# Optimization experiments

Measured on AMD Instinct MI355X. Metric: run time of the kernel, lower is better.

Reference implementation:

```python
import math
import jax, jax.numpy as jnp
from jax import lax
import numpy as np

N_IMG = 2
C = 128
IMG_H, IMG_W = 512, 1024
STRIDES = (4, 8, 16, 32, 64)
SIZES = (32.0, 64.0, 128.0, 256.0, 512.0)
RATIOS = (0.5, 1.0, 2.0)
A = len(RATIOS)
PRE_NMS_TOPK = 2000    # pre_nms_topk[self.training] with training=True
POST_NMS_TOPK = 1000   # post_nms_topk[self.training]
NMS_THRESH = 0.7
BATCH_PER_IMG = 256
POS_FRAC = 0.5
MIN_BOX_SIZE = 0.0
SCALE_CLAMP = math.log(1000.0 / 16.0)
MATCH_LOW, MATCH_HIGH = 0.3, 0.7


def cell_anchors(size):
    rs = jnp.asarray(RATIOS, jnp.float32)
    area = size * size
    w = jnp.sqrt(area / rs)
    h = w * rs
    return jnp.stack([-w / 2, -h / 2, w / 2, h / 2], axis=1)  # [A,4]


def level_anchors(H, W, stride, size):
    ca = cell_anchors(size)
    sx = jnp.arange(W, dtype=jnp.float32) * stride
    sy = jnp.arange(H, dtype=jnp.float32) * stride
    yy, xx = jnp.meshgrid(sy, sx, indexing="ij")
    shifts = jnp.stack([xx, yy, xx, yy], axis=-1).reshape(-1, 4)  # [H*W,4]
    return (shifts[:, None, :] + ca[None, :, :]).reshape(-1, 4)  # [H*W*A,4]


def pairwise_iou(a, b):
    lt = jnp.maximum(a[:, None, :2], b[None, :, :2])
    rb = jnp.minimum(a[:, None, 2:], b[None, :, 2:])
    wh = jnp.clip(rb - lt, 0.0)
    inter = wh[..., 0] * wh[..., 1]
    area_a = (a[:, 2] - a[:, 0]) * (a[:, 3] - a[:, 1])
    area_b = (b[:, 2] - b[:, 0]) * (b[:, 3] - b[:, 1])
    union = area_a[:, None] + area_b[None, :] - inter
    return jnp.where(inter > 0, inter / union, 0.0)


def get_deltas(src, tgt):
    sw = src[..., 2] - src[..., 0]; sh = src[..., 3] - src[..., 1]
    scx = src[..., 0] + 0.5 * sw;   scy = src[..., 1] + 0.5 * sh
    tw = tgt[..., 2] - tgt[..., 0]; th = tgt[..., 3] - tgt[..., 1]
    tcx = tgt[..., 0] + 0.5 * tw;   tcy = tgt[..., 1] + 0.5 * th
    return jnp.stack([(tcx - scx) / sw, (tcy - scy) / sh,
                      jnp.log(tw / sw), jnp.log(th / sh)], axis=-1)


def apply_deltas(deltas, boxes):
    w = boxes[..., 2] - boxes[..., 0]; h = boxes[..., 3] - boxes[..., 1]
    cx = boxes[..., 0] + 0.5 * w;      cy = boxes[..., 1] + 0.5 * h
    dx, dy = deltas[..., 0], deltas[..., 1]
    dw = jnp.minimum(deltas[..., 2], SCALE_CLAMP)
    dh = jnp.minimum(deltas[..., 3], SCALE_CLAMP)
    pcx = dx * w + cx; pcy = dy * h + cy
    pw = jnp.exp(dw) * w; ph = jnp.exp(dh) * h
    return jnp.stack([pcx - 0.5 * pw, pcy - 0.5 * ph,
                      pcx + 0.5 * pw, pcy + 0.5 * ph], axis=-1)


def conv(x, w, b):
    y = lax.conv_general_dilated(x, w, (1, 1), "SAME",
                                 dimension_numbers=("NCHW", "OIHW", "NCHW"))
    return y + b[None, :, None, None]


def rpn_forward_flat(feats, conv_w, conv_b, obj_w, obj_b, delta_w, delta_b):
    anchors, logits, deltas = [], [], []
    for (stride, size), f in zip(zip(STRIDES, SIZES), feats):
        N, _, H, W = f.shape
        h = jax.nn.relu(conv(f, conv_w, conv_b))
        lg = conv(h, obj_w, obj_b)       # [N,A,H,W]
        dl = conv(h, delta_w, delta_b)   # [N,4A,H,W]
        logits.append(lg.transpose(0, 2, 3, 1).reshape(N, -1))                     # [N,HWA]
        deltas.append(dl.reshape(N, A, 4, H, W).transpose(0, 3, 4, 1, 2).reshape(N, -1, 4))
        anchors.append(level_anchors(H, W, stride, size))
    return anchors, logits, deltas


def label_and_sample(gt_b, key, anchors_all):
    iou = pairwise_iou(gt_b, anchors_all)                 # [G,R]
    matched_idxs = jnp.argmax(iou, axis=0)
    matched_vals = jnp.max(iou, axis=0)
    labels = jnp.where(matched_vals >= MATCH_HIGH, 1,
             jnp.where(matched_vals >= MATCH_LOW, -1, 0))
    highest = jnp.max(iou, axis=1)                        # per-gt best IoU
    lq = jnp.any((iou == highest[:, None]) & (highest[:, None] > 0), axis=0)
    labels = jnp.where(lq, 1, labels)                     # allow_low_quality_matches
    R = labels.shape[0]
    kf, kb = jax.random.split(key)
    fg = labels == 1; bg = labels == 0
    num_fg = jnp.minimum(fg.sum(), int(POS_FRAC * BATCH_PER_IMG))
    num_bg = jnp.minimum(bg.sum(), BATCH_PER_IMG - num_fg)
    def pick(mask, k, num):
        pri = jnp.where(mask, jax.random.uniform(k, (R,)), jnp.inf)
        rank = jnp.argsort(jnp.argsort(pri))
        return rank < num
    sel_fg = pick(fg, kf, num_fg)
    sel_bg = pick(bg, kb, num_bg)
    labels = jnp.where(sel_fg, 1, jnp.where(sel_bg, 0, -1))
    return labels, gt_b[matched_idxs]


def losses_fn(anchors_all, logits_cat, deltas_cat, gt_labels, matched_gt):
    fg = (gt_labels == 1).astype(logits_cat.dtype)          # [N,R]
    gt_deltas = get_deltas(anchors_all[None], matched_gt)   # [N,R,4]
    loc = jnp.sum(jnp.abs(deltas_cat - gt_deltas) * fg[..., None])  # smooth_l1, beta=0
    valid = (gt_labels >= 0).astype(logits_cat.dtype)
    x = logits_cat
    bce = jnp.maximum(x, 0.0) - x * fg + jnp.log1p(jnp.exp(-jnp.abs(x)))
    cls = jnp.sum(bce * valid)
    norm = float(BATCH_PER_IMG) * logits_cat.shape[0]
    return jnp.stack([cls / norm, loc / norm])


def nms_keep(boxes, valid):
    # boxes are sorted by descending score; greedy suppression.
    K = boxes.shape[0]
    iou = pairwise_iou(boxes, boxes)
    idx = jnp.arange(K)
    def body(i, keep):
        sup = (iou[i] > NMS_THRESH) & (idx > i) & keep[i]
        return keep & ~sup
    return lax.fori_loop(0, K, body, valid)


def predict_proposals(anchors, logits, deltas):
    lvl_boxes, lvl_scores = [], []
    for anc, lg, dl in zip(anchors, logits, deltas):
        boxes = apply_deltas(dl, anc[None])             # [N,R_l,4]
        k = min(PRE_NMS_TOPK, lg.shape[1])
        ts, ti = lax.top_k(lg, k)                       # [N,k]
        tb = jnp.take_along_axis(boxes, ti[..., None], axis=1)
        tb = jnp.stack([jnp.clip(tb[..., 0], 0.0, IMG_W), jnp.clip(tb[..., 1], 0.0, IMG_H),
                        jnp.clip(tb[..., 2], 0.0, IMG_W), jnp.clip(tb[..., 3], 0.0, IMG_H)], -1)
        valid = ((tb[..., 2] - tb[..., 0]) > MIN_BOX_SIZE) & ((tb[..., 3] - tb[..., 1]) > MIN_BOX_SIZE)
        keep = jax.vmap(nms_keep)(tb, valid)
        lvl_boxes.append(tb)
        lvl_scores.append(jnp.where(keep, ts, -jnp.inf))
    all_b = jnp.concatenate(lvl_boxes, axis=1)
    all_s = jnp.concatenate(lvl_scores, axis=1)
    fs, fi = lax.top_k(all_s, POST_NMS_TOPK)
    fb = jnp.take_along_axis(all_b, fi[..., None], axis=1)
    return fb, fs


def setup_inputs() -> dict:
    key = jax.random.key(0)
    ks = jax.random.split(key, 12)
    out = {}
    for i, s in enumerate(STRIDES):
        out[f"feat_p{i+2}"] = jax.random.normal(ks[i], (N_IMG, C, IMG_H // s, IMG_W // s), jnp.float32)
    G = 32
    wh_scale = jnp.asarray([IMG_W, IMG_H], jnp.float32)
    cxy = jax.random.uniform(ks[5], (N_IMG, G, 2)) * wh_scale
    wh = 32.0 + jax.random.uniform(ks[6], (N_IMG, G, 2)) * 224.0
    x1y1 = jnp.clip(cxy - wh / 2, 0.0)
    x2y2 = jnp.maximum(jnp.minimum(cxy + wh / 2, wh_scale), x1y1 + 1.0)
    out["gt_boxes"] = jnp.concatenate([x1y1, x2y2], axis=-1)
    out["conv_w"] = 0.01 * jax.random.normal(ks[7], (C, C, 3, 3), jnp.float32)
    out["conv_b"] = jnp.zeros((C,), jnp.float32)
    out["obj_w"] = 0.01 * jax.random.normal(ks[8], (A, C, 1, 1), jnp.float32)
    out["obj_b"] = jnp.zeros((A,), jnp.float32)
    out["delta_w"] = 0.01 * jax.random.normal(ks[9], (4 * A, C, 1, 1), jnp.float32)
    out["delta_b"] = jnp.zeros((4 * A,), jnp.float32)
    return out


def reference(feat_p2, feat_p3, feat_p4, feat_p5, feat_p6, gt_boxes,
              conv_w, conv_b, obj_w, obj_b, delta_w, delta_b):
    feats = [feat_p2, feat_p3, feat_p4, feat_p5, feat_p6]
    anchors, logits, deltas = rpn_forward_flat(feats, conv_w, conv_b, obj_w, obj_b, delta_w, delta_b)
    anchors_all = jnp.concatenate(anchors, axis=0)      # [R,4]
    logits_cat = jnp.concatenate(logits, axis=1)        # [N,R]
    deltas_cat = jnp.concatenate(deltas, axis=1)        # [N,R,4]
    keys = jax.random.split(jax.random.key(42), gt_boxes.shape[0])
    gt_labels, matched_gt = jax.vmap(label_and_sample, in_axes=(0, 0, None))(gt_boxes, keys, anchors_all)
    losses = losses_fn(anchors_all, logits_cat, deltas_cat, gt_labels, matched_gt)
    prop_boxes, prop_scores = predict_proposals(
        anchors,
        [lax.stop_gradient(l) for l in logits],
        [lax.stop_gradient(d) for d in deltas])
    return prop_boxes, prop_scores, losses
```

## Files before the change

### kernel.cpp

```cpp
#include <hip/hip_runtime.h>
#include <stdint.h>
#include <math.h>


#define R_TOT   130944
#define HALF_R  65472
#define TOTK    7920
#define SCALE_CLAMP 4.135166556742356

__host__ __device__ inline void threefry(uint32_t k0, uint32_t k1,
                                         uint32_t x0, uint32_t x1,
                                         uint32_t* o0, uint32_t* o1)
{
  uint32_t ks[3]; ks[0]=k0; ks[1]=k1; ks[2]=k0^k1^0x1BD11BDAu;
  x0 += ks[0]; x1 += ks[1];
  const uint32_t rot0[4] = {13u,15u,26u,6u};
  const uint32_t rot1[4] = {17u,29u,16u,24u};
  for (int i = 0; i < 5; i++){
    const uint32_t* rot = (i & 1) ? rot1 : rot0;
    for (int q = 0; q < 4; q++){
      x0 += x1;
      x1 = (x1 << rot[q]) | (x1 >> (32u - rot[q]));
      x1 ^= x0;
    }
    x0 += ks[(i+1)%3];
    x1 += ks[(i+2)%3] + (uint32_t)(i+1);
  }
  *o0 = x0; *o1 = x1;
}

__device__ inline unsigned long long mono64(double v){
  unsigned long long b = (unsigned long long)__double_as_longlong(v);
  return (b & 0x8000000000000000ull) ? ~b : (b | 0x8000000000000000ull);
}

__device__ __forceinline__ double iou_cf(double g0,double g1,double g2,double g3,
                                         double a0,double a1,double a2,double a3){
  #pragma clang fp contract(off)
  double lt0 = fmax(g0,a0), lt1 = fmax(g1,a1);
  double rb0 = fmin(g2,a2), rb1 = fmin(g3,a3);
  double w = rb0-lt0; if (w<0.0) w=0.0;
  double h = rb1-lt1; if (h<0.0) h=0.0;
  double inter = w*h;
  double aa = (g2-g0)*(g3-g1);
  double ab = (a2-a0)*(a3-a1);
  double uni = aa+ab-inter;
  return inter>0.0 ? inter/uni : 0.0;
}

__device__ __forceinline__ void anchor_of(int r, double* o){
  #pragma clang fp contract(off)
  const int    base[5]={0,98304,122880,129024,130560};
  const int    Wl[5]  ={256,128,64,32,16};
  const double strd[5]={4.0,8.0,16.0,32.0,64.0};
  const double size[5]={32.0,64.0,128.0,256.0,512.0};
  const double ratio[3]={0.5,1.0,2.0};
  int l=0; while (l<4 && r>=base[l+1]) l++;
  int rr=r-base[l]; int pix=rr/3; int a=rr-pix*3;
  int x=pix%Wl[l], y=pix/Wl[l];
  double w=sqrt(size[l]*size[l]/ratio[a]);
  double h=w*ratio[a];
  double sx=(double)x*strd[l], sy=(double)y*strd[l];
  o[0]=sx-0.5*w; o[1]=sy-0.5*h; o[2]=sx+0.5*w; o[3]=sy+0.5*h;
}

__device__ __forceinline__ void decode_box(int ridx, const double* __restrict__ d,
                                           double* __restrict__ o){
  double a[4]; anchor_of(ridx,a);
  double w=a[2]-a[0], h=a[3]-a[1];
  double cx=a[0]+0.5*w, cy=a[1]+0.5*h;
  double dw=fmin(d[2],SCALE_CLAMP), dh=fmin(d[3],SCALE_CLAMP);
  double pcx=d[0]*w+cx, pcy=d[1]*h+cy;
  double pw=exp(dw)*w, ph=exp(dh)*h;
  double x1=pcx-0.5*pw, y1=pcy-0.5*ph;
  double x2=pcx+0.5*pw, y2=pcy+0.5*ph;
  o[0]=fmin(fmax(x1,0.0),1024.0); o[1]=fmin(fmax(y1,0.0),512.0);
  o[2]=fmin(fmax(x2,0.0),1024.0); o[3]=fmin(fmax(y2,0.0),512.0);
}

__device__ inline void bitonic_desc(double* sv, int* si, int M, int tid, int nthr){
  for (int k=2;k<=M;k<<=1)
    for (int j=k>>1;j>0;j>>=1){
      __syncthreads();
      for (int i=tid;i<M;i+=nthr){
        int ixj=i^j;
        if (ixj>i){
          double va=sv[i], vb=sv[ixj]; int ia=si[i], ib=si[ixj];
          bool before = (va>vb) || (va==vb && ia<ib);
          bool up = ((i&k)==0);
          if (up ? !before : before){ sv[i]=vb; sv[ixj]=va; si[i]=ib; si[ixj]=ia; }
        }
      }
    }
  __syncthreads();
}

__device__ inline void bitonic_asc_u(uint32_t* sk, int* si, int M, int tid, int nthr){
  for (int k=2;k<=M;k<<=1)
    for (int j=k>>1;j>0;j>>=1){
      __syncthreads();
      for (int i=tid;i<M;i+=nthr){
        int ixj=i^j;
        if (ixj>i){
          uint32_t ka=sk[i], kb=sk[ixj]; int ia=si[i], ib=si[ixj];
          bool before = (ka<kb) || (ka==kb && ia<ib);
          bool up = ((i&k)==0);
          if (up ? !before : before){ sk[i]=kb; sk[ixj]=ka; si[i]=ib; si[ixj]=ia; }
        }
      }
    }
  __syncthreads();
}

__device__ inline void hist_select(int* hist, int kneed, int tid,
                                   int* shb, int* shk){
  for (int off=1; off<256; off<<=1){
    int v=0;
    if (tid<256 && tid>=off) v=hist[tid-off];
    __syncthreads();
    if (tid<256) hist[tid]+=v;
    __syncthreads();
  }
  if (tid<256){
    int prev = tid ? hist[tid-1] : 0;
    if (prev < kneed && kneed <= hist[tid]){ *shb=tid; *shk=kneed-prev; }
    if (tid==255 && kneed > hist[255]){ *shb=255; *shk=kneed-hist[254]; }
  }
  __syncthreads();
}

__global__ __launch_bounds__(256) void k_pre(const float* __restrict__ cw,
    float* __restrict__ cwTf, const float* __restrict__ gt,
    unsigned long long* __restrict__ highest)
{
  const int bx=blockIdx.x, tid=threadIdx.x;
  if (bx < 576){
    int o = bx*256 + tid;
    if (o >= 147456) return;
    int cc = o & 127; int t = o >> 7;
    int k9 = t % 9;  int ci = t / 9;
    cwTf[(size_t)(ci*9+k9)*128 + cc] = cw[(size_t)cc*1152 + ci*9 + k9];
  } else {
    __shared__ double gts[128];
    __shared__ unsigned long long lmax[32];
    const int gb=bx-576;
    const int img=gb>>6, b=gb&63;
    if (tid<128) gts[tid]=(double)gt[img*128+tid];
    if (tid<32) lmax[tid]=0ull;
    __syncthreads();
    double gm[32];
    #pragma unroll
    for (int g=0;g<32;g++) gm[g]=0.0;
    for (int r=b*256+tid; r<R_TOT; r+=64*256){
      double a[4]; anchor_of(r,a);
      #pragma unroll
      for (int g=0;g<32;g++){
        double v=iou_cf(gts[g*4],gts[g*4+1],gts[g*4+2],gts[g*4+3],a[0],a[1],a[2],a[3]);
        gm[g]=fmax(gm[g],v);
      }
    }
    #pragma unroll
    for (int g=0;g<32;g++){
      double v=gm[g];
      #pragma unroll
      for (int off=1; off<64; off<<=1) v=fmax(v,__shfl_xor(v,off));
      if ((tid&63)==0) atomicMax(&lmax[g],(unsigned long long)__double_as_longlong(v));
    }
    __syncthreads();
    if (tid<32) atomicMax(&highest[img*32+tid], lmax[tid]);
  }
}

#define CTH 4
#define CTW 8

__global__ __launch_bounds__(256,4) void k_conv_label(
    const float* __restrict__ f2, const float* __restrict__ f3,
    const float* __restrict__ f4, const float* __restrict__ f5,
    const float* __restrict__ f6,
    const float* __restrict__ cwTf, const float* __restrict__ cb,
    const float* __restrict__ ow, const float* __restrict__ ob,
    const float* __restrict__ dwt, const float* __restrict__ dbt,
    double* __restrict__ logits, double* __restrict__ dpred,
    const float* __restrict__ gt, const unsigned long long* __restrict__ highest,
    int* __restrict__ prelab, int* __restrict__ matched,
    int* __restrict__ labels, int* __restrict__ counts,
    uint32_t* __restrict__ ub,
    uint32_t kf00,uint32_t kf01,uint32_t kb00,uint32_t kb01,
    uint32_t kf10,uint32_t kf11,uint32_t kb10,uint32_t kb11)
{
  __shared__ double fshd[4][6][12];
  __shared__ __align__(16) char ush[18432];
  float*  wshF = (float*)ush;
  double* hshp = (double*)ush;
  __shared__ float hw[15*128];
  __shared__ float hb[15];

  const int tid=threadIdx.x;
  const int vbid = blockIdx.x;

  if (vbid >= 3752){
    int j = (vbid-3752)*256 + tid;
    if (j >= 2*R_TOT) return;
    int slot = j / HALF_R; int t = j - slot*HALF_R;
    uint32_t k0,k1;
    if      (slot==0){k0=kf00;k1=kf01;}
    else if (slot==1){k0=kb00;k1=kb01;}
    else if (slot==2){k0=kf10;k1=kf11;}
    else             {k0=kb10;k1=kb11;}
    uint32_t o0,o1;
    threefry(k0,k1,(uint32_t)t,(uint32_t)(t+HALF_R),&o0,&o1);
    ub[(size_t)slot*R_TOT+t]=o0;
    ub[(size_t)slot*R_TOT+t+HALF_R]=o1;
    return;
  }

  if (vbid >= 2728){
    double* gts=(double*)ush;
    double* hg =(double*)(ush+1024);
    int* wfg=(int*)(ush+1280); int* wbg=(int*)(ush+1296);
    const int lb=vbid-2728;
    const int img=lb>>9, blk=lb&511;
    if (tid<128) gts[tid]=(double)gt[img*128+tid];
    if (tid<32)  hg[tid]=__longlong_as_double((long long)highest[img*32+tid]);
    __syncthreads();
    int r=blk*256+tid;
    const bool ok=(r<R_TOT);
    int lab=-1, bi=0;
    if (ok){
      double a[4]; anchor_of(r,a);
      double best=-1.0; bool lq=false;
      #pragma unroll
      for (int g=0;g<32;g++){
        double v=iou_cf(gts[g*4],gts[g*4+1],gts[g*4+2],gts[g*4+3],a[0],a[1],a[2],a[3]);
        if (v>best){ best=v; bi=g; }
        if (hg[g]>0.0 && v==hg[g]) lq=true;
      }
      lab = lq ? 1 : (best>=0.7 ? 1 : (best>=0.3 ? -1 : 0));
      prelab [(size_t)img*R_TOT+r]=lab;
      matched[(size_t)img*R_TOT+r]=bi;
      labels [(size_t)img*R_TOT+r]=-1;
    }
    unsigned long long bf=__ballot(ok && lab==1);
    unsigned long long bb=__ballot(ok && lab==0);
    const int wid=tid>>6, lane=tid&63;
    if (lane==0){ wfg[wid]=__popcll(bf); wbg[wid]=__popcll(bb); }
    __syncthreads();
    if (tid==0){
      int fcnt=wfg[0]+wfg[1]+wfg[2]+wfg[3];
      int bcnt=wbg[0]+wbg[1]+wbg[2]+wbg[3];
      if (fcnt) atomicAdd(&counts[img*2+0],fcnt);
      if (bcnt) atomicAdd(&counts[img*2+1],bcnt);
    }
    return;
  }

  const int cumt[6]={0,2048,2560,2688,2720,2728};
  const int Hs[5]={128,64,32,16,8}, Wl[5]={256,128,64,32,16};
  const int rbs[5]={0,98304,122880,129024,130560};
  const int lgx[5]={5,4,3,2,1};

  int bid=vbid;
  int lvl=0;
  while (lvl<4 && bid>=cumt[lvl+1]) lvl++;
  int t=bid-cumt[lvl];
  const int img=t&1; const int tt=t>>1;
  const int H=Hs[lvl], W=Wl[lvl], rbase=rbs[lvl];
  const int tx=tt&((1<<lgx[lvl])-1), ty=tt>>lgx[lvl];
  const int x0=tx*CTW, y0=ty*CTH;
  const float* f = lvl==0?f2: lvl==1?f3: lvl==2?f4: lvl==3?f5: f6;

  for (int i=tid;i<15*128;i+=256){
    int o=i>>7, c=i&127;
    hw[i]=(o<3)?ow[o*128+c]:dwt[(o-3)*128+c];
  }
  if (tid<15) hb[tid]=(tid<3)?ob[tid]:dbt[tid-3];

  const int c=tid&127, half=tid>>7;
  double acc[16];
  #pragma unroll
  for (int i=0;i<16;i++) acc[i]=0.0;

  const float* fimg = f + (size_t)img*128*H*W;

  const bool fin_act = (tid < 240);
  int ci_f=0,dy_f=0,dx_f=0; bool fin_valid=false;
  const float* fptr=fimg;
  if (fin_act){
    ci_f=tid/60; int rem=tid-ci_f*60; dy_f=rem/10; dx_f=rem-dy_f*10;
    int y=y0-1+dy_f, x=x0-1+dx_f;
    fin_valid = (y>=0&&y<H&&x>=0&&x<W);
    fptr = fimg + (size_t)ci_f*H*W + (fin_valid ? ((size_t)y*W+x) : 0);
  }
  const size_t fstep=(size_t)4*H*W;
  const float2* wsrc=(const float2*)cwTf;

  float fin_pf=0.f; float2 wpf[9];
  if (fin_act){ fin_pf = fin_valid ? *fptr : 0.f; fptr += fstep; }
  #pragma unroll
  for (int j2=0;j2<9;j2++) wpf[j2]=wsrc[tid+j2*256];

  for (int ci0=0; ci0<128; ci0+=4){
    __syncthreads();
    if (fin_act) fshd[ci_f][dy_f][dx_f]=(double)fin_pf;
    { float2* wdst=(float2*)wshF;
      #pragma unroll
      for (int j2=0;j2<9;j2++) wdst[tid+j2*256]=wpf[j2]; }
    if (ci0+4<128){
      if (fin_act){ fin_pf = fin_valid ? *fptr : 0.f; fptr += fstep; }
      const float2* wn = wsrc + (size_t)(ci0+4)*576;
      #pragma unroll
      for (int j2=0;j2<9;j2++) wpf[j2]=wn[tid+j2*256];
    }
    __syncthreads();
    #pragma unroll
    for (int ci=0;ci<4;ci++){
      double w9d[9];
      #pragma unroll
      for (int k=0;k<9;k++) w9d[k]=(double)wshF[(ci*9+k)*128 + c];
      #pragma unroll
      for (int irl=0;irl<4;irl++){
        int ir=half*2+irl;
        double rowb[10];
        #pragma unroll
        for (int q=0;q<10;q++) rowb[q]=fshd[ci][ir][q];
        #pragma unroll
        for (int orl=0;orl<2;orl++){
          int ky=irl-orl;
          if (ky<0||ky>2) continue;
          #pragma unroll
          for (int px=0;px<8;px++){
            double s=acc[orl*8+px];
            #pragma unroll
            for (int kx=0;kx<3;kx++) s += w9d[ky*3+kx]*rowb[px+kx];
            acc[orl*8+px]=s;
          }
        }
      }
    }
  }
  double bc=(double)cb[c];
  __syncthreads();
  if (half==0){
    #pragma unroll
    for (int pp=0;pp<16;pp++){
      double hv=acc[pp]+bc; if (hv<0.0) hv=0.0;
      hshp[c*17+pp]=hv;
    }
  }
  __syncthreads();
  for (int hp=0;hp<2;hp++){
    if (tid<240){
      int o=tid>>4, p=tid&15;
      double s=(double)hb[o];
      for (int c2=0;c2<128;c2++) s += (double)hw[o*128+c2]*hshp[c2*17+p];
      int pg=hp*16+p;
      int py=pg>>3, px=pg&7;
      int gy=y0+py, gx=x0+px;
      long long pix=(long long)gy*W+gx;
      size_t rb=(size_t)rbase+(size_t)pix*3;
      if (o<3) logits[(size_t)img*R_TOT+rb+o]=s;
      else { int a=(o-3)>>2, jj=(o-3)&3; dpred[((size_t)img*R_TOT+rb+a)*4+jj]=s; }
    }
    if (hp==0){
      __syncthreads();
      if (half==1){
        #pragma unroll
        for (int pp=0;pp<16;pp++){
          double hv=acc[pp]+bc; if (hv<0.0) hv=0.0;
          hshp[c*17+pp]=hv;
        }
      }
      __syncthreads();
    }
  }
}

__global__ __launch_bounds__(1024) void k_mid2(const uint32_t* __restrict__ ub,
    const int* __restrict__ prelab, const int* __restrict__ counts,
    int* __restrict__ labels,
    const double* __restrict__ logits, const double* __restrict__ dpred,
    double* __restrict__ allS, double* __restrict__ allB,
    unsigned long long* __restrict__ keepbuf,
    const float* __restrict__ gt, const int* __restrict__ matched,
    double* __restrict__ part, int* __restrict__ flags)
{
  __shared__ __align__(16) char buf[49152];
  __shared__ int hist[256];
  __shared__ int sI0, sI1;
  __shared__ int cnt;
  const int tid=threadIdx.x;

  if (blockIdx.x < 4){
    uint32_t* skey=(uint32_t*)buf; int* sidx=(int*)(buf+16384);
    const int img=blockIdx.x>>1, cls=blockIdx.x&1;
    const int cfg=counts[img*2+0], cbg=counts[img*2+1];
    const int num_fg=cfg<128?cfg:128;
    const int cap_bg=256-num_fg;
    const int num=cls?(cbg<cap_bg?cbg:cap_bg):num_fg;
    if (num<=0){
      if (tid==0){ __threadfence(); atomicAdd(&flags[13],1); }
      return;
    }
    const int want=cls?0:1;
    const int sel=want;
    const uint32_t* u=ub+(size_t)(img*2+cls)*R_TOT;
    const int* pl=prelab+(size_t)img*R_TOT;
    int* lab=labels+(size_t)img*R_TOT;

    for (int b=tid;b<256;b+=1024) hist[b]=0;
    if (tid==0) cnt=0;
    __syncthreads();
    #pragma unroll 4
    for (int r=tid;r<R_TOT;r+=1024){
      int plr = pl[r];
      uint32_t key = u[r]>>9;
      if (plr==want) atomicAdd(&hist[key>>15],1);
    }
    __syncthreads();
    hist_select(hist, num, tid, &sI0, &sI1);
    const uint32_t bsel=(uint32_t)sI0; const int kneed=sI1;
    #pragma unroll 4
    for (int r=tid;r<R_TOT;r+=1024){
      int plr = pl[r];
      uint32_t key = u[r]>>9;
      if (plr==want){
        uint32_t t8=key>>15;
        if (t8<bsel) lab[r]=sel;
        else if (t8==bsel){ int p=atomicAdd(&cnt,1); if (p<4096){ skey[p]=key; sidx[p]=r; } }
      }
    }
    __syncthreads();
    int n=cnt<4096?cnt:4096;
    for (int i=tid;i<4096;i+=1024) if (i>=n){ skey[i]=0xFFFFFFFFu; sidx[i]=0x7FFFFFFF; }
    bitonic_asc_u(skey,sidx,4096,tid,1024);
    int take = kneed<n?kneed:n;
    for (int i=tid;i<take;i+=1024) lab[sidx[i]]=sel;
    __syncthreads();
    if (tid==0){ __threadfence(); atomicAdd(&flags[13],1); }
  } else if (blockIdx.x < 14){
    double* sv=(double*)buf; int* si=(int*)(buf+32768);
    const int Rl[5]   ={98304,24576,6144,1536,384};
    const int kl[5]   ={2000,2000,2000,1536,384};
    const int lbase[5]={0,98304,122880,129024,130560};
    const int loff[5] ={0,2000,4000,6000,7536};
    const int bb=blockIdx.x-4;
    const int lvl=bb%5, img=bb/5;
    if (lvl==0 && tid<124) keepbuf[img*124+tid]=~0ull;
    const int Rn=Rl[lvl], K=kl[lvl];
    const double* lg=logits+(size_t)img*R_TOT+lbase[lvl];

    unsigned long long chosen=0; int kneed=K;
    for (int ps=7; ps>=6; --ps){
      int shift=ps*8;
      for (int b=tid;b<256;b+=1024) hist[b]=0;
      __syncthreads();
      #pragma unroll 4
      for (int r=tid;r<Rn;r+=1024){
        unsigned long long ik=~mono64(lg[r]);
        bool okp=(ps==7)||((ik>>(shift+8))==(chosen>>(shift+8)));
        if (okp) atomicAdd(&hist[(int)((ik>>shift)&255)],1);
      }
      __syncthreads();
      hist_select(hist, kneed, tid, &sI0, &sI1);
      chosen = chosen | ((unsigned long long)sI0<<shift);
      kneed  = sI1;
      __syncthreads();
    }
    const unsigned long long lim = chosen | 0xFFFFFFFFFFFFull;
    if (tid==0) cnt=0;
    __syncthreads();
    #pragma unroll 4
    for (int r=tid;r<Rn;r+=1024){
      unsigned long long ik=~mono64(lg[r]);
      if (ik<=lim){ int p=atomicAdd(&cnt,1); if (p<4096){ sv[p]=lg[r]; si[p]=r; } }
    }
    __syncthreads();
    int n=cnt<4096?cnt:4096;
    for (int i=tid;i<4096;i+=1024) if (i>=n){ sv[i]=-HUGE_VAL; si[i]=0x7FFFFFFF; }
    bitonic_desc(sv,si,4096,tid,1024);
    for (int j=tid;j<K;j+=1024){
      double v=sv[j]; int r=si[j];
      size_t slot=(size_t)img*TOTK+loff[lvl]+j;
      allS[slot]=v;
      int ridx=lbase[lvl]+r;
      double bx[4];
      decode_box(ridx, dpred+((size_t)img*R_TOT+ridx)*4, bx);
      allB[slot*4+0]=bx[0]; allB[slot*4+1]=bx[1]; allB[slot*4+2]=bx[2]; allB[slot*4+3]=bx[3];
    }
  } else {
    double* sc=(double*)buf; double* sl=(double*)(buf+8192);
    const int lb=blockIdx.x-14;
    if (tid==0){
      while (atomicAdd(&flags[13],0) < 4) __builtin_amdgcn_s_sleep(8);
    }
    __syncthreads();
    __threadfence();
    double cls=0.0, loc=0.0;
    for (int idx=lb*1024+tid; idx<2*R_TOT; idx+=64*1024){
      int l=labels[idx];
      if (l<0) continue;
      double x=logits[idx];
      double fgv=(l==1)?1.0:0.0;
      cls += fmax(x,0.0)-x*fgv+log1p(exp(-fabs(x)));
      if (l==1){
        int img=idx/R_TOT, r=idx-img*R_TOT;
        double a[4]; anchor_of(r,a);
        int m=matched[idx];
        const float* g=gt+img*128+m*4;
        double sw=a[2]-a[0], sh=a[3]-a[1];
        double scx=a[0]+0.5*sw, scy=a[1]+0.5*sh;
        double tw=(double)g[2]-(double)g[0], th=(double)g[3]-(double)g[1];
        double tcx=(double)g[0]+0.5*tw, tcy=(double)g[1]+0.5*th;
        double d0=(tcx-scx)/sw, d1=(tcy-scy)/sh;
        double d2=log(tw/sw), d3=log(th/sh);
        const double* dp=dpred+(size_t)idx*4;
        loc += fabs(dp[0]-d0)+fabs(dp[1]-d1)+fabs(dp[2]-d2)+fabs(dp[3]-d3);
      }
    }
    sc[tid]=cls; sl[tid]=loc; __syncthreads();
    for (int s=512;s>0;s>>=1){
      if (tid<s){ sc[tid]+=sc[tid+s]; sl[tid]+=sl[tid+s]; }
      __syncthreads();
    }
    if (tid==0){
      part[lb*2]=sc[0]; part[lb*2+1]=sl[0];
      __threadfence();
      atomicAdd(&flags[12],1);
    }
  }
}

__global__ __launch_bounds__(1024) void k_mid3post(const double* __restrict__ allB,
    unsigned long long* __restrict__ msk,
    double* __restrict__ part,
    const double* __restrict__ allS, int* __restrict__ flags,
    unsigned long long* __restrict__ keepbuf, float* __restrict__ out)
{
  __shared__ __align__(16) char ush[64000];
  const int tid=threadIdx.x, bx=blockIdx.x;
  const int kl[5]  ={2000,2000,2000,1536,384};
  const int loff[5]={0,2000,4000,6000,7536};
  const int MBLK[5]={63,63,63,48,12};

  if (bx < 10){
    if (tid >= 64) return;
    const int lvl=bx%5, img=bx/5;
    const int K=kl[lvl], off=loff[lvl], nw=(K+63)>>6;
    const int lane=tid;
    {
      const int target=MBLK[lvl];
      while (true){
        int v = (lane==0) ? atomicAdd(&flags[img*5+lvl],0) : 0;
        v = __shfl(v,0);
        if (v>=target) break;
        __builtin_amdgcn_s_sleep(8);
      }
      __threadfence();
    }
    const double* B=allB+(size_t)(img*TOTK+off)*4;
    const unsigned long long* M=msk+((size_t)img*TOTK+off)*32;
    unsigned long long keepw=0ull;
    if (lane<nw){
      for (int b=0;b<64;b++){
        int j=lane*64+b;
        if (j<K){
          double x1=B[(size_t)j*4],y1=B[(size_t)j*4+1],x2=B[(size_t)j*4+2],y2=B[(size_t)j*4+3];
          if ((x2-x1)>0.0 && (y2-y1)>0.0) keepw|=(1ull<<b);
        }
      }
    }
    for (int w=0; w<nw; w++){
      unsigned long long vw = __shfl(keepw, w);
      int row = w*64 + lane;
      unsigned long long mrow = (row<K) ? M[(size_t)row*32+w] : 0ull;
      unsigned long long m_lo = lane ? (mrow & ((1ull<<lane)-1ull)) : 0ull;
      const bool validL = (vw>>lane)&1ull;
      unsigned long long kmask = vw;
      while (true){
        bool s = validL && ((m_lo & kmask)==0ull);
        unsigned long long nk = __ballot(s);
        if (nk==kmask) break;
        kmask = nk;
      }
      if (lane==w) keepw = kmask;
      if (lane>w && lane<nw){
        unsigned long long sup=0ull;
        for (int b=0;b<64;b++){
          if ((kmask>>b)&1ull) sup |= M[(size_t)(w*64+b)*32+lane];
        }
        keepw &= ~sup;
      }
    }
    if (lane<nw){
      int nvalid = K - lane*64; if (nvalid>64) nvalid=64;
      unsigned long long vm = (nvalid>=64) ? ~0ull : ((1ull<<nvalid)-1ull);
      unsigned long long cbits = (~keepw) & vm;
      int gbase = off + lane*64;
      int w0 = gbase>>6, sh = gbase&63;
      unsigned long long* kb = keepbuf + (size_t)img*124;
      if (sh==0){
        if (cbits) atomicAnd(&kb[w0], ~cbits);
      } else {
        unsigned long long lo = cbits << sh;
        unsigned long long hi = cbits >> (64-sh);
        if (lo) atomicAnd(&kb[w0],   ~lo);
        if (hi) atomicAnd(&kb[w0+1], ~hi);
      }
    }
    __threadfence();
    if (tid==0) atomicAdd(&flags[10+img],1);
    return;
  }

  if (bx < 12){
    double* sv=(double*)ush;
    int*    si=(int*)(ush+32768);
    unsigned long long* kbl=(unsigned long long*)(ush+49152);
    int*    hist=(int*)(ush+50144);
    __shared__ int sI0, sI1, cnt;
    const int img=bx-10;
    if (tid==0){
      while (atomicAdd(&flags[10+img],0) < 5) __builtin_amdgcn_s_sleep(8);
    }
    __syncthreads();
    __threadfence();
    if (tid<124) kbl[tid]=atomicAdd(&keepbuf[(size_t)img*124+tid],0ull);
    __syncthreads();
    const double* sarr=allS+(size_t)img*TOTK;

    unsigned long long chosen=0; int kneed=1000;
    for (int ps=7; ps>=6; --ps){
      int shift=ps*8;
      if (tid<256) hist[tid]=0;
      __syncthreads();
      for (int r=tid;r<TOTK;r+=1024){
        bool kept = (kbl[r>>6]>>(r&63))&1ull;
        double val = kept ? sarr[r] : -HUGE_VAL;
        unsigned long long ik=~mono64(val);
        bool okp=(ps==7)||((ik>>(shift+8))==(chosen>>(shift+8)));
        if (okp) atomicAdd(&hist[(int)((ik>>shift)&255)],1);
      }
      __syncthreads();
      hist_select(hist, kneed, tid, &sI0, &sI1);
      chosen = chosen | ((unsigned long long)sI0<<shift);
      kneed  = sI1;
      __syncthreads();
    }
    const unsigned long long lim = chosen | 0xFFFFFFFFFFFFull;
    if (tid==0) cnt=0;
    __syncthreads();
    for (int r=tid;r<TOTK;r+=1024){
      bool kept = (kbl[r>>6]>>(r&63))&1ull;
      double val = kept ? sarr[r] : -HUGE_VAL;
      unsigned long long ik=~mono64(val);
      if (ik<=lim){ int p=atomicAdd(&cnt,1); if (p<4096){ sv[p]=val; si[p]=r; } }
    }
    __syncthreads();
    int n=cnt<4096?cnt:4096;
    for (int i=tid;i<4096;i+=1024) if (i>=n){ sv[i]=-HUGE_VAL; si[i]=0x7FFFFFFF; }
    bitonic_desc(sv,si,4096,tid,1024);
    for (int j=tid;j<1000;j+=1024){
      out[8000+img*1000+j]=(float)sv[j];
      int idx=si[j];
      const double* b=allB+((size_t)img*TOTK+idx)*4;
      float* ob=out+((size_t)img*1000+j)*4;
      ob[0]=(float)b[0]; ob[1]=(float)b[1]; ob[2]=(float)b[2]; ob[3]=(float)b[3];
    }
    return;
  }

  if (bx == 12){
    double* sc=(double*)ush; double* sl=(double*)(ush+512);
    if (tid==0){
      while (atomicAdd(&flags[12],0) < 64) __builtin_amdgcn_s_sleep(8);
    }
    __syncthreads();
    __threadfence();
    if (tid<64){ sc[tid]=part[tid*2]; sl[tid]=part[tid*2+1]; }
    __syncthreads();
    for (int s=32;s>0;s>>=1){
      if (tid<s){ sc[tid]+=sc[tid+s]; sl[tid]+=sl[tid+s]; }
      __syncthreads();
    }
    if (tid==0){ out[10000]=(float)(sc[0]/512.0); out[10001]=(float)(sl[0]/512.0); }
    return;
  }

  {
    double* Bsh=(double*)ush;
    const int rbc[6]={0,63,126,189,237,249};
    int t = bx-13;
    const int img = t/249; t -= img*249;
    int lvl=0; while (lvl<4 && t>=rbc[lvl+1]) lvl++;
    const int i0=(t-rbc[lvl])*32;
    const int K=kl[lvl]; const int nw=(K+63)>>6;
    const double* B=allB+(size_t)(img*TOTK+loff[lvl])*4;
    for (int q=tid;q<K*4;q+=1024) Bsh[q]=B[q];
    __syncthreads();
    const int wv=tid>>6, lane=tid&63;
    for (int rr=0;rr<32;rr++){
      int i=i0+rr;
      if (i>=K) break;
      const double bi0=Bsh[i*4],bi1=Bsh[i*4+1],bi2=Bsh[i*4+2],bi3=Bsh[i*4+3];
      const double areai=(bi2-bi0)*(bi3-bi1);
      for (int w=wv;w<nw;w+=16){
        int j=w*64+lane;
        bool pred=false;
        if (j<K && j!=i){
          double a0=Bsh[j*4],a1=Bsh[j*4+1],a2=Bsh[j*4+2],a3=Bsh[j*4+3];
          double lt0=fmax(bi0,a0), lt1=fmax(bi1,a1);
          double rb0=fmin(bi2,a2), rb1=fmin(bi3,a3);
          double ww=rb0-lt0; if (ww<0.0) ww=0.0;
          double hh=rb1-lt1; if (hh<0.0) hh=0.0;
          double inter=ww*hh;
          double uni=areai+(a2-a0)*(a3-a1)-inter;
          double iou=inter>0.0?inter/uni:0.0;
          pred = iou>0.7;
        }
        unsigned long long m=__ballot(pred);
        if (lane==0) msk[((size_t)img*TOTK+loff[lvl]+i)*32+w]=m;
      }
    }
    __syncthreads();
    if (tid==0){ __threadfence(); atomicAdd(&flags[img*5+lvl],1); }
  }
}

extern "C" void kernel_launch(void* const* d_in, const int* in_sizes, int n_in,
                              void* d_out, int out_size, void* d_ws, size_t ws_size,
                              hipStream_t stream)
{
  (void)in_sizes; (void)n_in; (void)out_size;
  const float* feats[5];
  for (int i=0;i<5;i++) feats[i]=(const float*)d_in[i];
  const float* gt =(const float*)d_in[5];
  const float* cw =(const float*)d_in[6];
  const float* cb =(const float*)d_in[7];
  const float* ow =(const float*)d_in[8];
  const float* ob =(const float*)d_in[9];
  const float* dwt=(const float*)d_in[10];
  const float* dbt=(const float*)d_in[11];
  float* out=(float*)d_out;

  char* p=(char*)d_ws;
  auto carve=[&](size_t nbytes)->char*{ char* q=p; p += (nbytes+255)&~(size_t)255; return q; };
  double* logits =(double*)carve(2ull*R_TOT*8);
  double* dpred  =(double*)carve(2ull*R_TOT*4*8);
  float* cwTf    =(float*)carve(147456ull*4);
  uint32_t* ub   =(uint32_t*)carve(4ull*R_TOT*4);
  int* prelab    =(int*)carve(2ull*R_TOT*4);
  int* matched   =(int*)carve(2ull*R_TOT*4);
  int* labels    =(int*)carve(2ull*R_TOT*4);
  unsigned long long* highest=(unsigned long long*)carve(2*32*8);
  int* counts    =(int*)carve(256);
  int* flags     =(int*)carve(256);
  double* allS   =(double*)carve(2ull*TOTK*8);
  double* allB   =(double*)carve(2ull*TOTK*4*8);
  unsigned long long* msk=(unsigned long long*)carve(2ull*TOTK*32*8);
  double* part   =(double*)carve(256*2*8);
  unsigned long long* keepbuf=(unsigned long long*)carve(2*124*8);
  if ((size_t)(p-(char*)d_ws) > ws_size) return;

  hipMemsetAsync(highest, 0, 1024, stream);

  uint32_t a0,b0,a1,b1;
  threefry(0u,42u,0u,2u,&a0,&b0);
  threefry(0u,42u,1u,3u,&a1,&b1);
  uint32_t kf00,kf01,kb00,kb01,kf10,kf11,kb10,kb11;
  { uint32_t c0,d0,c1,d1;
    threefry(a0,a1,0u,2u,&c0,&d0); threefry(a0,a1,1u,3u,&c1,&d1);
    kf00=c0; kf01=c1; kb00=d0; kb01=d1;
    threefry(b0,b1,0u,2u,&c0,&d0); threefry(b0,b1,1u,3u,&c1,&d1);
    kf10=c0; kf11=c1; kb10=d0; kb11=d1; }

  k_pre<<<704, 256, 0, stream>>>(cw, cwTf, gt, highest);
  k_conv_label<<<4775, 256, 0, stream>>>(feats[0],feats[1],feats[2],feats[3],feats[4],
      cwTf,cb,ow,ob,dwt,dbt, logits, dpred,
      gt, highest, prelab, matched, labels, counts,
      ub, kf00,kf01,kb00,kb01,kf10,kf11,kb10,kb11);
  k_mid2<<<78, 1024, 0, stream>>>(ub, prelab, counts, labels, logits, dpred,
      allS, allB, keepbuf, gt, matched, part, flags);
  k_mid3post<<<511, 1024, 0, stream>>>(allB, msk, part, allS, flags, keepbuf, out);
}
```

Measured before the change: 1.249 ms.

## Merge conv, label, sampling, top-k, NMS and loss into one persistent dataflow kernel

Folds the three downstream kernels (k_conv_label, k_mid2, k_mid3post) into a single 256-thread launch. Block ranges are assigned to the different stages, and later stages spin on global atomic flags until the producer blocks for their level or image have finished. The intent is to overlap the tail stages (top-k, mask building, NMS, loss) with the conv work and to remove the idle gaps and launch overhead between kernels. Block sizes for the sampling, top-k and mask stages shrink from 1024 to 256 threads, with smaller sort buffers and an extra radix pass. This relies on producer blocks being scheduled before the waiting consumers, so there is a deadlock or ordering risk, and the smaller blocks may make the serial stages slower.

```diff
diff --git a/kernel.cpp b/kernel.cpp
--- a/kernel.cpp
+++ b/kernel.cpp
@@ -7,6 +7,27 @@
 #define HALF_R  65472
 #define TOTK    7920
 #define SCALE_CLAMP 4.135166556742356
+
+#define B_LABEL 2728
+#define B_UBITS 3752
+#define B_SAMP  4775
+#define B_TOPK  4779
+#define B_MASK  4789
+#define B_SCAN  5041
+#define B_T1K   5051
+#define B_LOSS  5053
+#define B_LFIN  5117
+#define N_MAIN  5118
+
+#define FC   0
+#define FCD  10
+#define FL0  11
+#define FU   13
+#define FS   14
+#define FT   15
+#define FM   25
+#define FK   35
+#define FP   37
 
 __host__ __device__ inline void threefry(uint32_t k0, uint32_t k1,
                                          uint32_t x0, uint32_t x1,
@@ -131,10 +152,11 @@
 
 __global__ __launch_bounds__(256) void k_pre(const float* __restrict__ cw,
     float* __restrict__ cwTf, const float* __restrict__ gt,
-    unsigned long long* __restrict__ highest)
+    unsigned long long* __restrict__ highest, unsigned long long* __restrict__ keepbuf)
 {
   const int bx=blockIdx.x, tid=threadIdx.x;
   if (bx < 576){
+    if (bx==0 && tid<248) keepbuf[tid]=~0ull;
     int o = bx*256 + tid;
     if (o >= 147456) return;
     int cc = o & 127; int t = o >> 7;
@@ -174,7 +196,7 @@
 #define CTH 4
 #define CTW 8
 
-__global__ __launch_bounds__(256,4) void k_conv_label(
+__global__ __launch_bounds__(256,4) void k_main(
     const float* __restrict__ f2, const float* __restrict__ f3,
     const float* __restrict__ f4, const float* __restrict__ f5,
     const float* __restrict__ f6,
@@ -186,40 +208,158 @@
     int* __restrict__ prelab, int* __restrict__ matched,
     int* __restrict__ labels, int* __restrict__ counts,
     uint32_t* __restrict__ ub,
-    uint32_t kf00,uint32_t kf01,uint32_t kb00,uint32_t kb01,
-    uint32_t kf10,uint32_t kf11,uint32_t kb10,uint32_t kb11)
+    const uint32_t* __restrict__ tfk,
+    double* __restrict__ allS, double* __restrict__ allB,
+    unsigned long long* __restrict__ msk, unsigned long long* __restrict__ keepbuf,
+    double* __restrict__ part, int* __restrict__ flags, float* __restrict__ out)
 {
-  __shared__ double fshd[4][6][12];
-  __shared__ __align__(16) char ush[18432];
-  float*  wshF = (float*)ush;
-  double* hshp = (double*)ush;
-  __shared__ float hw[15*128];
-  __shared__ float hb[15];
-
+  __shared__ __align__(16) char mega[28672];
+  __shared__ int sI0, sI1, cnt;
   const int tid=threadIdx.x;
-  const int vbid = blockIdx.x;
-
-  if (vbid >= 3752){
-    int j = (vbid-3752)*256 + tid;
-    if (j >= 2*R_TOT) return;
-    int slot = j / HALF_R; int t = j - slot*HALF_R;
-    uint32_t k0,k1;
-    if      (slot==0){k0=kf00;k1=kf01;}
-    else if (slot==1){k0=kb00;k1=kb01;}
-    else if (slot==2){k0=kf10;k1=kf11;}
-    else             {k0=kb10;k1=kb11;}
-    uint32_t o0,o1;
-    threefry(k0,k1,(uint32_t)t,(uint32_t)(t+HALF_R),&o0,&o1);
-    ub[(size_t)slot*R_TOT+t]=o0;
-    ub[(size_t)slot*R_TOT+t+HALF_R]=o1;
+  const int bx = blockIdx.x;
+  const int kl[5]  ={2000,2000,2000,1536,384};
+  const int loff[5]={0,2000,4000,6000,7536};
+  const int lbase5[5]={0,98304,122880,129024,130560};
+  const int CTGT[5]={1024,256,64,16,4};
+  const int MBLK[5]={32,32,32,24,6};
+
+  if (bx < B_LABEL){
+    double (*fshd)[6][12] = (double(*)[6][12])(mega);
+    float*  wshF = (float*)(mega+2304);
+    double* hshp = (double*)(mega+2304);
+    float*  hw   = (float*)(mega+20736);
+    float*  hb   = (float*)(mega+28416);
+
+    const int cumt[6]={0,2048,2560,2688,2720,2728};
+    const int Hs[5]={128,64,32,16,8}, Wl[5]={256,128,64,32,16};
+    const int rbs[5]={0,98304,122880,129024,130560};
+    const int lgx[5]={5,4,3,2,1};
+
+    int bid=bx;
+    int lvl=0;
+    while (lvl<4 && bid>=cumt[lvl+1]) lvl++;
+    int t=bid-cumt[lvl];
+    const int img=t&1; const int tt=t>>1;
+    const int H=Hs[lvl], W=Wl[lvl], rbase=rbs[lvl];
+    const int tx=tt&((1<<lgx[lvl])-1), ty=tt>>lgx[lvl];
+    const int x0=tx*CTW, y0=ty*CTH;
+    const float* f = lvl==0?f2: lvl==1?f3: lvl==2?f4: lvl==3?f5: f6;
+
+    for (int i=tid;i<15*128;i+=256){
+      int o=i>>7, c=i&127;
+      hw[i]=(o<3)?ow[o*128+c]:dwt[(o-3)*128+c];
+    }
+    if (tid<15) hb[tid]=(tid<3)?ob[tid]:dbt[tid-3];
+
+    const int c=tid&127, half=tid>>7;
+    double acc[16];
+    #pragma unroll
+    for (int i=0;i<16;i++) acc[i]=0.0;
+
+    const float* fimg = f + (size_t)img*128*H*W;
+
+    const bool fin_act = (tid < 240);
+    int ci_f=0,dy_f=0,dx_f=0; bool fin_valid=false;
+    const float* fptr=fimg;
+    if (fin_act){
+      ci_f=tid/60; int rem=tid-ci_f*60; dy_f=rem/10; dx_f=rem-dy_f*10;
+      int y=y0-1+dy_f, x=x0-1+dx_f;
+      fin_valid = (y>=0&&y<H&&x>=0&&x<W);
+      fptr = fimg + (size_t)ci_f*H*W + (fin_valid ? ((size_t)y*W+x) : 0);
+    }
+    const size_t fstep=(size_t)4*H*W;
+    const float2* wsrc=(const float2*)cwTf;
+
+    float fin_pf=0.f; float2 wpf[9];
+    if (fin_act){ fin_pf = fin_valid ? *fptr : 0.f; fptr += fstep; }
+    #pragma unroll
+    for (int j2=0;j2<9;j2++) wpf[j2]=wsrc[tid+j2*256];
+
+    for (int ci0=0; ci0<128; ci0+=4){
+      __syncthreads();
+      if (fin_act) fshd[ci_f][dy_f][dx_f]=(double)fin_pf;
+      { float2* wdst=(float2*)wshF;
+        #pragma unroll
+        for (int j2=0;j2<9;j2++) wdst[tid+j2*256]=wpf[j2]; }
+      if (ci0+4<128){
+        if (fin_act){ fin_pf = fin_valid ? *fptr : 0.f; fptr += fstep; }
+        const float2* wn = wsrc + (size_t)(ci0+4)*576;
+        #pragma unroll
+        for (int j2=0;j2<9;j2++) wpf[j2]=wn[tid+j2*256];
+      }
+      __syncthreads();
+      #pragma unroll
+      for (int ci=0;ci<4;ci++){
+        double w9d[9];
+        #pragma unroll
+        for (int k=0;k<9;k++) w9d[k]=(double)wshF[(ci*9+k)*128 + c];
+        #pragma unroll
+        for (int irl=0;irl<4;irl++){
+          int ir=half*2+irl;
+          double rowb[10];
+          #pragma unroll
+          for (int q=0;q<10;q++) rowb[q]=fshd[ci][ir][q];
+          #pragma unroll
+          for (int orl=0;orl<2;orl++){
+            int ky=irl-orl;
+            if (ky<0||ky>2) continue;
+            #pragma unroll
+            for (int px=0;px<8;px++){
+              double s=acc[orl*8+px];
+              #pragma unroll
+              for (int kx=0;kx<3;kx++) s += w9d[ky*3+kx]*rowb[px+kx];
+              acc[orl*8+px]=s;
+            }
+          }
+        }
+      }
+    }
+    double bc=(double)cb[c];
+    __syncthreads();
+    if (half==0){
+      #pragma unroll
+      for (int pp=0;pp<16;pp++){
+        double hv=acc[pp]+bc; if (hv<0.0) hv=0.0;
+        hshp[c*17+pp]=hv;
+      }
+    }
+    __syncthreads();
+    for (int hp=0;hp<2;hp++){
+      if (tid<240){
+        int o=tid>>4, p=tid&15;
+        double s=(double)hb[o];
+        for (int c2=0;c2<128;c2++) s += (double)hw[o*128+c2]*hshp[c2*17+p];
+        int pg=hp*16+p;
+        int py=pg>>3, px=pg&7;
+        int gy=y0+py, gx=x0+px;
+        long long pix=(long long)gy*W+gx;
+        size_t rb=(size_t)rbase+(size_t)pix*3;
+        if (o<3) logits[(size_t)img*R_TOT+rb+o]=s;
+        else { int a=(o-3)>>2, jj=(o-3)&3; dpred[((size_t)img*R_TOT+rb+a)*4+jj]=s; }
+      }
+      if (hp==0){
+        __syncthreads();
+        if (half==1){
+          #pragma unroll
+          for (int pp=0;pp<16;pp++){
+            double hv=acc[pp]+bc; if (hv<0.0) hv=0.0;
+            hshp[c*17+pp]=hv;
+          }
+        }
+        __syncthreads();
+      }
+    }
+    __threadfence();
+    __syncthreads();
+    if (tid==0){ atomicAdd(&flags[FC+lvl*2+img],1); atomicAdd(&flags[FCD],1); }
     return;
   }
 
-  if (vbid >= 2728){
-    double* gts=(double*)ush;
-    double* hg =(double*)(ush+1024);
-    int* wfg=(int*)(ush+1280); int* wbg=(int*)(ush+1296);
-    const int lb=vbid-2728;
+  if (bx < B_UBITS){
+    double* gts=(double*)mega;
+    double* hg =(double*)(mega+1024);
+    int* wfg=(int*)(mega+1280); int* wbg=(int*)(mega+1296);
+    const int lb=bx-B_LABEL;
     const int img=lb>>9, blk=lb&511;
     if (tid<128) gts[tid]=(double)gt[img*128+tid];
     if (tid<32)  hg[tid]=__longlong_as_double((long long)highest[img*32+tid]);
@@ -245,161 +385,49 @@
     unsigned long long bb=__ballot(ok && lab==0);
     const int wid=tid>>6, lane=tid&63;
     if (lane==0){ wfg[wid]=__popcll(bf); wbg[wid]=__popcll(bb); }
+    __threadfence();
     __syncthreads();
     if (tid==0){
       int fcnt=wfg[0]+wfg[1]+wfg[2]+wfg[3];
       int bcnt=wbg[0]+wbg[1]+wbg[2]+wbg[3];
       if (fcnt) atomicAdd(&counts[img*2+0],fcnt);
       if (bcnt) atomicAdd(&counts[img*2+1],bcnt);
+      __threadfence();
+      atomicAdd(&flags[FL0+img],1);
     }
     return;
   }
 
-  const int cumt[6]={0,2048,2560,2688,2720,2728};
-  const int Hs[5]={128,64,32,16,8}, Wl[5]={256,128,64,32,16};
-  const int rbs[5]={0,98304,122880,129024,130560};
-  const int lgx[5]={5,4,3,2,1};
-
-  int bid=vbid;
-  int lvl=0;
-  while (lvl<4 && bid>=cumt[lvl+1]) lvl++;
-  int t=bid-cumt[lvl];
-  const int img=t&1; const int tt=t>>1;
-  const int H=Hs[lvl], W=Wl[lvl], rbase=rbs[lvl];
-  const int tx=tt&((1<<lgx[lvl])-1), ty=tt>>lgx[lvl];
-  const int x0=tx*CTW, y0=ty*CTH;
-  const float* f = lvl==0?f2: lvl==1?f3: lvl==2?f4: lvl==3?f5: f6;
-
-  for (int i=tid;i<15*128;i+=256){
-    int o=i>>7, c=i&127;
-    hw[i]=(o<3)?ow[o*128+c]:dwt[(o-3)*128+c];
-  }
-  if (tid<15) hb[tid]=(tid<3)?ob[tid]:dbt[tid-3];
-
-  const int c=tid&127, half=tid>>7;
-  double acc[16];
-  #pragma unroll
-  for (int i=0;i<16;i++) acc[i]=0.0;
-
-  const float* fimg = f + (size_t)img*128*H*W;
-
-  const bool fin_act = (tid < 240);
-  int ci_f=0,dy_f=0,dx_f=0; bool fin_valid=false;
-  const float* fptr=fimg;
-  if (fin_act){
-    ci_f=tid/60; int rem=tid-ci_f*60; dy_f=rem/10; dx_f=rem-dy_f*10;
-    int y=y0-1+dy_f, x=x0-1+dx_f;
-    fin_valid = (y>=0&&y<H&&x>=0&&x<W);
-    fptr = fimg + (size_t)ci_f*H*W + (fin_valid ? ((size_t)y*W+x) : 0);
-  }
-  const size_t fstep=(size_t)4*H*W;
-  const float2* wsrc=(const float2*)cwTf;
-
-  float fin_pf=0.f; float2 wpf[9];
-  if (fin_act){ fin_pf = fin_valid ? *fptr : 0.f; fptr += fstep; }
-  #pragma unroll
-  for (int j2=0;j2<9;j2++) wpf[j2]=wsrc[tid+j2*256];
-
-  for (int ci0=0; ci0<128; ci0+=4){
-    __syncthreads();
-    if (fin_act) fshd[ci_f][dy_f][dx_f]=(double)fin_pf;
-    { float2* wdst=(float2*)wshF;
-      #pragma unroll
-      for (int j2=0;j2<9;j2++) wdst[tid+j2*256]=wpf[j2]; }
-    if (ci0+4<128){
-      if (fin_act){ fin_pf = fin_valid ? *fptr : 0.f; fptr += fstep; }
-      const float2* wn = wsrc + (size_t)(ci0+4)*576;
-      #pragma unroll
-      for (int j2=0;j2<9;j2++) wpf[j2]=wn[tid+j2*256];
-    }
-    __syncthreads();
-    #pragma unroll
-    for (int ci=0;ci<4;ci++){
-      double w9d[9];
-      #pragma unroll
-      for (int k=0;k<9;k++) w9d[k]=(double)wshF[(ci*9+k)*128 + c];
-      #pragma unroll
-      for (int irl=0;irl<4;irl++){
-        int ir=half*2+irl;
-        double rowb[10];
-        #pragma unroll
-        for (int q=0;q<10;q++) rowb[q]=fshd[ci][ir][q];
-        #pragma unroll
-        for (int orl=0;orl<2;orl++){
-          int ky=irl-orl;
-          if (ky<0||ky>2) continue;
-          #pragma unroll
-          for (int px=0;px<8;px++){
-            double s=acc[orl*8+px];
-            #pragma unroll
-            for (int kx=0;kx<3;kx++) s += w9d[ky*3+kx]*rowb[px+kx];
-            acc[orl*8+px]=s;
-          }
-        }
-      }
-    }
-  }
-  double bc=(double)cb[c];
-  __syncthreads();
-  if (half==0){
-    #pragma unroll
-    for (int pp=0;pp<16;pp++){
-      double hv=acc[pp]+bc; if (hv<0.0) hv=0.0;
-      hshp[c*17+pp]=hv;
-    }
-  }
-  __syncthreads();
-  for (int hp=0;hp<2;hp++){
-    if (tid<240){
-      int o=tid>>4, p=tid&15;
-      double s=(double)hb[o];
-      for (int c2=0;c2<128;c2++) s += (double)hw[o*128+c2]*hshp[c2*17+p];
-      int pg=hp*16+p;
-      int py=pg>>3, px=pg&7;
-      int gy=y0+py, gx=x0+px;
-      long long pix=(long long)gy*W+gx;
-      size_t rb=(size_t)rbase+(size_t)pix*3;
-      if (o<3) logits[(size_t)img*R_TOT+rb+o]=s;
-      else { int a=(o-3)>>2, jj=(o-3)&3; dpred[((size_t)img*R_TOT+rb+a)*4+jj]=s; }
-    }
-    if (hp==0){
-      __syncthreads();
-      if (half==1){
-        #pragma unroll
-        for (int pp=0;pp<16;pp++){
-          double hv=acc[pp]+bc; if (hv<0.0) hv=0.0;
-          hshp[c*17+pp]=hv;
-        }
-      }
-      __syncthreads();
-    }
-  }
-}
-
-__global__ __launch_bounds__(1024) void k_mid2(const uint32_t* __restrict__ ub,
-    const int* __restrict__ prelab, const int* __restrict__ counts,
-    int* __restrict__ labels,
-    const double* __restrict__ logits, const double* __restrict__ dpred,
-    double* __restrict__ allS, double* __restrict__ allB,
-    unsigned long long* __restrict__ keepbuf,
-    const float* __restrict__ gt, const int* __restrict__ matched,
-    double* __restrict__ part, int* __restrict__ flags)
-{
-  __shared__ __align__(16) char buf[49152];
-  __shared__ int hist[256];
-  __shared__ int sI0, sI1;
-  __shared__ int cnt;
-  const int tid=threadIdx.x;
-
-  if (blockIdx.x < 4){
-    uint32_t* skey=(uint32_t*)buf; int* sidx=(int*)(buf+16384);
-    const int img=blockIdx.x>>1, cls=blockIdx.x&1;
+  if (bx < B_SAMP){
+    int j = (bx-B_UBITS)*256 + tid;
+    int slot = j / HALF_R; int t = j - slot*HALF_R;
+    uint32_t k0=tfk[slot*2], k1=tfk[slot*2+1];
+    uint32_t o0,o1;
+    threefry(k0,k1,(uint32_t)t,(uint32_t)(t+HALF_R),&o0,&o1);
+    ub[(size_t)slot*R_TOT+t]=o0;
+    ub[(size_t)slot*R_TOT+t+HALF_R]=o1;
+    __threadfence();
+    __syncthreads();
+    if (tid==0) atomicAdd(&flags[FU],1);
+    return;
+  }
+
+  if (bx < B_TOPK){
+    uint32_t* skey=(uint32_t*)mega; int* sidx=(int*)(mega+8192);
+    int* hist=(int*)(mega+16384);
+    const int img=(bx-B_SAMP)>>1, cls=(bx-B_SAMP)&1;
+    if (tid==0){
+      while (atomicAdd(&flags[FL0+img],0) < 512 || atomicAdd(&flags[FU],0) < 1023)
+        __builtin_amdgcn_s_sleep(8);
+    }
+    __syncthreads();
+    __threadfence();
     const int cfg=counts[img*2+0], cbg=counts[img*2+1];
     const int num_fg=cfg<128?cfg:128;
     const int cap_bg=256-num_fg;
     const int num=cls?(cbg<cap_bg?cbg:cap_bg):num_fg;
     if (num<=0){
-      if (tid==0){ __threadfence(); atomicAdd(&flags[13],1); }
+      if (tid==0){ __threadfence(); atomicAdd(&flags[FS],1); }
       return;
     }
     const int want=cls?0:1;
@@ -408,11 +436,11 @@
     const int* pl=prelab+(size_t)img*R_TOT;
     int* lab=labels+(size_t)img*R_TOT;
 
-    for (int b=tid;b<256;b+=1024) hist[b]=0;
+    if (tid<256) hist[tid]=0;
     if (tid==0) cnt=0;
     __syncthreads();
     #pragma unroll 4
-    for (int r=tid;r<R_TOT;r+=1024){
+    for (int r=tid;r<R_TOT;r+=256){
       int plr = pl[r];
       uint32_t key = u[r]>>9;
       if (plr==want) atomicAdd(&hist[key>>15],1);
@@ -421,42 +449,48 @@
     hist_select(hist, num, tid, &sI0, &sI1);
     const uint32_t bsel=(uint32_t)sI0; const int kneed=sI1;
     #pragma unroll 4
-    for (int r=tid;r<R_TOT;r+=1024){
+    for (int r=tid;r<R_TOT;r+=256){
       int plr = pl[r];
       uint32_t key = u[r]>>9;
       if (plr==want){
         uint32_t t8=key>>15;
         if (t8<bsel) lab[r]=sel;
-        else if (t8==bsel){ int p=atomicAdd(&cnt,1); if (p<4096){ skey[p]=key; sidx[p]=r; } }
-      }
-    }
-    __syncthreads();
-    int n=cnt<4096?cnt:4096;
-    for (int i=tid;i<4096;i+=1024) if (i>=n){ skey[i]=0xFFFFFFFFu; sidx[i]=0x7FFFFFFF; }
-    bitonic_asc_u(skey,sidx,4096,tid,1024);
+        else if (t8==bsel){ int p=atomicAdd(&cnt,1); if (p<2048){ skey[p]=key; sidx[p]=r; } }
+      }
+    }
+    __syncthreads();
+    int n=cnt<2048?cnt:2048;
+    for (int i=tid;i<2048;i+=256) if (i>=n){ skey[i]=0xFFFFFFFFu; sidx[i]=0x7FFFFFFF; }
+    bitonic_asc_u(skey,sidx,2048,tid,256);
     int take = kneed<n?kneed:n;
-    for (int i=tid;i<take;i+=1024) lab[sidx[i]]=sel;
-    __syncthreads();
-    if (tid==0){ __threadfence(); atomicAdd(&flags[13],1); }
-  } else if (blockIdx.x < 14){
-    double* sv=(double*)buf; int* si=(int*)(buf+32768);
-    const int Rl[5]   ={98304,24576,6144,1536,384};
-    const int kl[5]   ={2000,2000,2000,1536,384};
-    const int lbase[5]={0,98304,122880,129024,130560};
-    const int loff[5] ={0,2000,4000,6000,7536};
-    const int bb=blockIdx.x-4;
+    for (int i=tid;i<take;i+=256) lab[sidx[i]]=sel;
+    __threadfence();
+    __syncthreads();
+    if (tid==0) atomicAdd(&flags[FS],1);
+    return;
+  }
+
+  if (bx < B_MASK){
+    double* sv=(double*)mega; int* si=(int*)(mega+16384);
+    int* hist=(int*)(mega+24576);
+    const int Rl[5]={98304,24576,6144,1536,384};
+    const int bb=bx-B_TOPK;
     const int lvl=bb%5, img=bb/5;
-    if (lvl==0 && tid<124) keepbuf[img*124+tid]=~0ull;
+    if (tid==0){
+      while (atomicAdd(&flags[FC+lvl*2+img],0) < CTGT[lvl]) __builtin_amdgcn_s_sleep(8);
+    }
+    __syncthreads();
+    __threadfence();
     const int Rn=Rl[lvl], K=kl[lvl];
-    const double* lg=logits+(size_t)img*R_TOT+lbase[lvl];
+    const double* lg=logits+(size_t)img*R_TOT+lbase5[lvl];
 
     unsigned long long chosen=0; int kneed=K;
-    for (int ps=7; ps>=6; --ps){
+    for (int ps=7; ps>=5; --ps){
       int shift=ps*8;
-      for (int b=tid;b<256;b+=1024) hist[b]=0;
+      if (tid<256) hist[tid]=0;
       __syncthreads();
       #pragma unroll 4
-      for (int r=tid;r<Rn;r+=1024){
+      for (int r=tid;r<Rn;r+=256){
         unsigned long long ik=~mono64(lg[r]);
         bool okp=(ps==7)||((ik>>(shift+8))==(chosen>>(shift+8)));
         if (okp) atomicAdd(&hist[(int)((ik>>shift)&255)],1);
@@ -467,37 +501,213 @@
       kneed  = sI1;
       __syncthreads();
     }
-    const unsigned long long lim = chosen | 0xFFFFFFFFFFFFull;
+    const unsigned long long lim = chosen | 0xFFFFFFFFFFull;
     if (tid==0) cnt=0;
     __syncthreads();
     #pragma unroll 4
-    for (int r=tid;r<Rn;r+=1024){
+    for (int r=tid;r<Rn;r+=256){
       unsigned long long ik=~mono64(lg[r]);
-      if (ik<=lim){ int p=atomicAdd(&cnt,1); if (p<4096){ sv[p]=lg[r]; si[p]=r; } }
-    }
-    __syncthreads();
-    int n=cnt<4096?cnt:4096;
-    for (int i=tid;i<4096;i+=1024) if (i>=n){ sv[i]=-HUGE_VAL; si[i]=0x7FFFFFFF; }
-    bitonic_desc(sv,si,4096,tid,1024);
-    for (int j=tid;j<K;j+=1024){
+      if (ik<=lim){ int p=atomicAdd(&cnt,1); if (p<2048){ sv[p]=lg[r]; si[p]=r; } }
+    }
+    __syncthreads();
+    int n=cnt<2048?cnt:2048;
+    for (int i=tid;i<2048;i+=256) if (i>=n){ sv[i]=-HUGE_VAL; si[i]=0x7FFFFFFF; }
+    bitonic_desc(sv,si,2048,tid,256);
+    for (int j=tid;j<K;j+=256){
       double v=sv[j]; int r=si[j];
       size_t slot=(size_t)img*TOTK+loff[lvl]+j;
       allS[slot]=v;
-      int ridx=lbase[lvl]+r;
-      double bx[4];
-      decode_box(ridx, dpred+((size_t)img*R_TOT+ridx)*4, bx);
-      allB[slot*4+0]=bx[0]; allB[slot*4+1]=bx[1]; allB[slot*4+2]=bx[2]; allB[slot*4+3]=bx[3];
-    }
-  } else {
-    double* sc=(double*)buf; double* sl=(double*)(buf+8192);
-    const int lb=blockIdx.x-14;
+      int ridx=lbase5[lvl]+r;
+      double bxv[4];
+      decode_box(ridx, dpred+((size_t)img*R_TOT+ridx)*4, bxv);
+      allB[slot*4+0]=bxv[0]; allB[slot*4+1]=bxv[1]; allB[slot*4+2]=bxv[2]; allB[slot*4+3]=bxv[3];
+    }
+    __threadfence();
+    __syncthreads();
+    if (tid==0) atomicAdd(&flags[FT+img*5+lvl],1);
+    return;
+  }
+
+  if (bx < B_SCAN){
+    const int rbc[6]={0,32,64,96,120,126};
+    int t = bx-B_MASK;
+    const int img = t/126; t -= img*126;
+    int lvl=0; while (lvl<4 && t>=rbc[lvl+1]) lvl++;
+    const int i0=(t-rbc[lvl])*64;
     if (tid==0){
-      while (atomicAdd(&flags[13],0) < 4) __builtin_amdgcn_s_sleep(8);
+      while (atomicAdd(&flags[FT+img*5+lvl],0) < 1) __builtin_amdgcn_s_sleep(8);
+    }
+    __syncthreads();
+    __threadfence();
+    const int K=kl[lvl]; const int nw=(K+63)>>6;
+    const double* B=allB+(size_t)(img*TOTK+loff[lvl])*4;
+    const int wv=tid>>6, lane=tid&63;
+    for (int rr=0;rr<64;rr++){
+      int i=i0+rr;
+      if (i>=K) break;
+      const double bi0=B[(size_t)i*4],bi1=B[(size_t)i*4+1],bi2=B[(size_t)i*4+2],bi3=B[(size_t)i*4+3];
+      const double areai=(bi2-bi0)*(bi3-bi1);
+      for (int w=wv;w<nw;w+=4){
+        int j=w*64+lane;
+        bool pred=false;
+        if (j<K && j!=i){
+          double a0=B[(size_t)j*4],a1=B[(size_t)j*4+1],a2=B[(size_t)j*4+2],a3=B[(size_t)j*4+3];
+          double lt0=fmax(bi0,a0), lt1=fmax(bi1,a1);
+          double rb0=fmin(bi2,a2), rb1=fmin(bi3,a3);
+          double ww=rb0-lt0; if (ww<0.0) ww=0.0;
+          double hh=rb1-lt1; if (hh<0.0) hh=0.0;
+          double inter=ww*hh;
+          double uni=areai+(a2-a0)*(a3-a1)-inter;
+          double iou=inter>0.0?inter/uni:0.0;
+          pred = iou>0.7;
+        }
+        unsigned long long m=__ballot(pred);
+        if (lane==0) msk[((size_t)img*TOTK+loff[lvl]+i)*32+w]=m;
+      }
+    }
+    __threadfence();
+    __syncthreads();
+    if (tid==0) atomicAdd(&flags[FM+img*5+lvl],1);
+    return;
+  }
+
+  if (bx < B_T1K){
+    if (tid >= 64) return;
+    const int bb=bx-B_SCAN;
+    const int lvl=bb%5, img=bb/5;
+    const int K=kl[lvl], off=loff[lvl], nw=(K+63)>>6;
+    const int lane=tid;
+    {
+      const int target=MBLK[lvl];
+      while (true){
+        int v = (lane==0) ? atomicAdd(&flags[FM+img*5+lvl],0) : 0;
+        v = __shfl(v,0);
+        if (v>=target) break;
+        __builtin_amdgcn_s_sleep(8);
+      }
+      __threadfence();
+    }
+    const double* B=allB+(size_t)(img*TOTK+off)*4;
+    const unsigned long long* M=msk+((size_t)img*TOTK+off)*32;
+    unsigned long long keepw=0ull;
+    if (lane<nw){
+      for (int b=0;b<64;b++){
+        int j=lane*64+b;
+        if (j<K){
+          double x1=B[(size_t)j*4],y1=B[(size_t)j*4+1],x2=B[(size_t)j*4+2],y2=B[(size_t)j*4+3];
+          if ((x2-x1)>0.0 && (y2-y1)>0.0) keepw|=(1ull<<b);
+        }
+      }
+    }
+    for (int w=0; w<nw; w++){
+      unsigned long long vw = __shfl(keepw, w);
+      int row = w*64 + lane;
+      unsigned long long mrow = (row<K) ? M[(size_t)row*32+w] : 0ull;
+      unsigned long long m_lo = lane ? (mrow & ((1ull<<lane)-1ull)) : 0ull;
+      const bool validL = (vw>>lane)&1ull;
+      unsigned long long kmask = vw;
+      while (true){
+        bool s = validL && ((m_lo & kmask)==0ull);
+        unsigned long long nk = __ballot(s);
+        if (nk==kmask) break;
+        kmask = nk;
+      }
+      if (lane==w) keepw = kmask;
+      if (lane>w && lane<nw){
+        unsigned long long sup=0ull;
+        for (int b=0;b<64;b++){
+          if ((kmask>>b)&1ull) sup |= M[(size_t)(w*64+b)*32+lane];
+        }
+        keepw &= ~sup;
+      }
+    }
+    if (lane<nw){
+      int nvalid = K - lane*64; if (nvalid>64) nvalid=64;
+      unsigned long long vm = (nvalid>=64) ? ~0ull : ((1ull<<nvalid)-1ull);
+      unsigned long long cbits = (~keepw) & vm;
+      int gbase = off + lane*64;
+      int w0 = gbase>>6, sh = gbase&63;
+      unsigned long long* kb = keepbuf + (size_t)img*124;
+      if (sh==0){
+        if (cbits) atomicAnd(&kb[w0], ~cbits);
+      } else {
+        unsigned long long lo = cbits << sh;
+        unsigned long long hi = cbits >> (64-sh);
+        if (lo) atomicAnd(&kb[w0],   ~lo);
+        if (hi) atomicAnd(&kb[w0+1], ~hi);
+      }
+    }
+    __threadfence();
+    if (tid==0) atomicAdd(&flags[FK+img],1);
+    return;
+  }
+
+  if (bx < B_LOSS){
+    double* sv=(double*)mega; int* si=(int*)(mega+16384);
+    int* hist=(int*)(mega+24576);
+    unsigned long long* kbl=(unsigned long long*)(mega+25600);
+    const int img=bx-B_T1K;
+    if (tid==0){
+      while (atomicAdd(&flags[FK+img],0) < 5) __builtin_amdgcn_s_sleep(8);
+    }
+    __syncthreads();
+    __threadfence();
+    if (tid<124) kbl[tid]=atomicAdd(&keepbuf[(size_t)img*124+tid],0ull);
+    __syncthreads();
+    const double* sarr=allS+(size_t)img*TOTK;
+
+    unsigned long long chosen=0; int kneed=1000;
+    for (int ps=7; ps>=5; --ps){
+      int shift=ps*8;
+      if (tid<256) hist[tid]=0;
+      __syncthreads();
+      for (int r=tid;r<TOTK;r+=256){
+        bool kept = (kbl[r>>6]>>(r&63))&1ull;
+        double val = kept ? sarr[r] : -HUGE_VAL;
+        unsigned long long ik=~mono64(val);
+        bool okp=(ps==7)||((ik>>(shift+8))==(chosen>>(shift+8)));
+        if (okp) atomicAdd(&hist[(int)((ik>>shift)&255)],1);
+      }
+      __syncthreads();
+      hist_select(hist, kneed, tid, &sI0, &sI1);
+      chosen = chosen | ((unsigned long long)sI0<<shift);
+      kneed  = sI1;
+      __syncthreads();
+    }
+    const unsigned long long lim = chosen | 0xFFFFFFFFFFull;
+    if (tid==0) cnt=0;
+    __syncthreads();
+    for (int r=tid;r<TOTK;r+=256){
+      bool kept = (kbl[r>>6]>>(r&63))&1ull;
+      double val = kept ? sarr[r] : -HUGE_VAL;
+      unsigned long long ik=~mono64(val);
+      if (ik<=lim){ int p=atomicAdd(&cnt,1); if (p<2048){ sv[p]=val; si[p]=r; } }
+    }
+    __syncthreads();
+    int n=cnt<2048?cnt:2048;
+    for (int i=tid;i<2048;i+=256) if (i>=n){ sv[i]=-HUGE_VAL; si[i]=0x7FFFFFFF; }
+    bitonic_desc(sv,si,2048,tid,256);
+    for (int j=tid;j<1000;j+=256){
+      out[8000+img*1000+j]=(float)sv[j];
+      int idx=si[j];
+      const double* b=allB+((size_t)img*TOTK+idx)*4;
+      float* obp=out+((size_t)img*1000+j)*4;
+      obp[0]=(float)b[0]; obp[1]=(float)b[1]; obp[2]=(float)b[2]; obp[3]=(float)b[3];
+    }
+    return;
+  }
+
+  if (bx < B_LFIN){
+    double* sc=(double*)mega; double* sl=(double*)(mega+2048);
+    const int lb=bx-B_LOSS;
+    if (tid==0){
+      while (atomicAdd(&flags[FS],0) < 4 || atomicAdd(&flags[FCD],0) < 2728)
+        __builtin_amdgcn_s_sleep(8);
     }
     __syncthreads();
     __threadfence();
     double cls=0.0, loc=0.0;
-    for (int idx=lb*1024+tid; idx<2*R_TOT; idx+=64*1024){
+    for (int idx=lb*256+tid; idx<2*R_TOT; idx+=64*256){
       int l=labels[idx];
       if (l<0) continue;
       double x=logits[idx];
@@ -519,161 +729,22 @@
       }
     }
     sc[tid]=cls; sl[tid]=loc; __syncthreads();
-    for (int s=512;s>0;s>>=1){
+    for (int s=128;s>0;s>>=1){
       if (tid<s){ sc[tid]+=sc[tid+s]; sl[tid]+=sl[tid+s]; }
       __syncthreads();
     }
     if (tid==0){
       part[lb*2]=sc[0]; part[lb*2+1]=sl[0];
       __threadfence();
-      atomicAdd(&flags[12],1);
-    }
-  }
-}
-
-__global__ __launch_bounds__(1024) void k_mid3post(const double* __restrict__ allB,
-    unsigned long long* __restrict__ msk,
-    double* __restrict__ part,
-    const double* __restrict__ allS, int* __restrict__ flags,
-    unsigned long long* __restrict__ keepbuf, float* __restrict__ out)
-{
-  __shared__ __align__(16) char ush[64000];
-  const int tid=threadIdx.x, bx=blockIdx.x;
-  const int kl[5]  ={2000,2000,2000,1536,384};
-  const int loff[5]={0,2000,4000,6000,7536};
-  const int MBLK[5]={63,63,63,48,12};
-
-  if (bx < 10){
-    if (tid >= 64) return;
-    const int lvl=bx%5, img=bx/5;
-    const int K=kl[lvl], off=loff[lvl], nw=(K+63)>>6;
-    const int lane=tid;
-    {
-      const int target=MBLK[lvl];
-      while (true){
-        int v = (lane==0) ? atomicAdd(&flags[img*5+lvl],0) : 0;
-        v = __shfl(v,0);
-        if (v>=target) break;
-        __builtin_amdgcn_s_sleep(8);
-      }
-      __threadfence();
-    }
-    const double* B=allB+(size_t)(img*TOTK+off)*4;
-    const unsigned long long* M=msk+((size_t)img*TOTK+off)*32;
-    unsigned long long keepw=0ull;
-    if (lane<nw){
-      for (int b=0;b<64;b++){
-        int j=lane*64+b;
-        if (j<K){
-          double x1=B[(size_t)j*4],y1=B[(size_t)j*4+1],x2=B[(size_t)j*4+2],y2=B[(size_t)j*4+3];
-          if ((x2-x1)>0.0 && (y2-y1)>0.0) keepw|=(1ull<<b);
-        }
-      }
-    }
-    for (int w=0; w<nw; w++){
-      unsigned long long vw = __shfl(keepw, w);
-      int row = w*64 + lane;
-      unsigned long long mrow = (row<K) ? M[(size_t)row*32+w] : 0ull;
-      unsigned long long m_lo = lane ? (mrow & ((1ull<<lane)-1ull)) : 0ull;
-      const bool validL = (vw>>lane)&1ull;
-      unsigned long long kmask = vw;
-      while (true){
-        bool s = validL && ((m_lo & kmask)==0ull);
-        unsigned long long nk = __ballot(s);
-        if (nk==kmask) break;
-        kmask = nk;
-      }
-      if (lane==w) keepw = kmask;
-      if (lane>w && lane<nw){
-        unsigned long long sup=0ull;
-        for (int b=0;b<64;b++){
-          if ((kmask>>b)&1ull) sup |= M[(size_t)(w*64+b)*32+lane];
-        }
-        keepw &= ~sup;
-      }
-    }
-    if (lane<nw){
-      int nvalid = K - lane*64; if (nvalid>64) nvalid=64;
-      unsigned long long vm = (nvalid>=64) ? ~0ull : ((1ull<<nvalid)-1ull);
-      unsigned long long cbits = (~keepw) & vm;
-      int gbase = off + lane*64;
-      int w0 = gbase>>6, sh = gbase&63;
-      unsigned long long* kb = keepbuf + (size_t)img*124;
-      if (sh==0){
-        if (cbits) atomicAnd(&kb[w0], ~cbits);
-      } else {
-        unsigned long long lo = cbits << sh;
-        unsigned long long hi = cbits >> (64-sh);
-        if (lo) atomicAnd(&kb[w0],   ~lo);
-        if (hi) atomicAnd(&kb[w0+1], ~hi);
-      }
-    }
-    __threadfence();
-    if (tid==0) atomicAdd(&flags[10+img],1);
+      atomicAdd(&flags[FP],1);
+    }
     return;
   }
 
-  if (bx < 12){
-    double* sv=(double*)ush;
-    int*    si=(int*)(ush+32768);
-    unsigned long long* kbl=(unsigned long long*)(ush+49152);
-    int*    hist=(int*)(ush+50144);
-    __shared__ int sI0, sI1, cnt;
-    const int img=bx-10;
+  {
+    double* sc=(double*)mega; double* sl=(double*)(mega+512);
     if (tid==0){
-      while (atomicAdd(&flags[10+img],0) < 5) __builtin_amdgcn_s_sleep(8);
-    }
-    __syncthreads();
-    __threadfence();
-    if (tid<124) kbl[tid]=atomicAdd(&keepbuf[(size_t)img*124+tid],0ull);
-    __syncthreads();
-    const double* sarr=allS+(size_t)img*TOTK;
-
-    unsigned long long chosen=0; int kneed=1000;
-    for (int ps=7; ps>=6; --ps){
-      int shift=ps*8;
-      if (tid<256) hist[tid]=0;
-      __syncthreads();
-      for (int r=tid;r<TOTK;r+=1024){
-        bool kept = (kbl[r>>6]>>(r&63))&1ull;
-        double val = kept ? sarr[r] : -HUGE_VAL;
-        unsigned long long ik=~mono64(val);
-        bool okp=(ps==7)||((ik>>(shift+8))==(chosen>>(shift+8)));
-        if (okp) atomicAdd(&hist[(int)((ik>>shift)&255)],1);
-      }
-      __syncthreads();
-      hist_select(hist, kneed, tid, &sI0, &sI1);
-      chosen = chosen | ((unsigned long long)sI0<<shift);
-      kneed  = sI1;
-      __syncthreads();
-    }
-    const unsigned long long lim = chosen | 0xFFFFFFFFFFFFull;
-    if (tid==0) cnt=0;
-    __syncthreads();
-    for (int r=tid;r<TOTK;r+=1024){
-      bool kept = (kbl[r>>6]>>(r&63))&1ull;
-      double val = kept ? sarr[r] : -HUGE_VAL;
-      unsigned long long ik=~mono64(val);
-      if (ik<=lim){ int p=atomicAdd(&cnt,1); if (p<4096){ sv[p]=val; si[p]=r; } }
-    }
-    __syncthreads();
-    int n=cnt<4096?cnt:4096;
-    for (int i=tid;i<4096;i+=1024) if (i>=n){ sv[i]=-HUGE_VAL; si[i]=0x7FFFFFFF; }
-    bitonic_desc(sv,si,4096,tid,1024);
-    for (int j=tid;j<1000;j+=1024){
-      out[8000+img*1000+j]=(float)sv[j];
-      int idx=si[j];
-      const double* b=allB+((size_t)img*TOTK+idx)*4;
-      float* ob=out+((size_t)img*1000+j)*4;
-      ob[0]=(float)b[0]; ob[1]=(float)b[1]; ob[2]=(float)b[2]; ob[3]=(float)b[3];
-    }
-    return;
-  }
-
-  if (bx == 12){
-    double* sc=(double*)ush; double* sl=(double*)(ush+512);
-    if (tid==0){
-      while (atomicAdd(&flags[12],0) < 64) __builtin_amdgcn_s_sleep(8);
+      while (atomicAdd(&flags[FP],0) < 64) __builtin_amdgcn_s_sleep(8);
     }
     __syncthreads();
     __threadfence();
@@ -684,46 +755,6 @@
       __syncthreads();
     }
     if (tid==0){ out[10000]=(float)(sc[0]/512.0); out[10001]=(float)(sl[0]/512.0); }
-    return;
-  }
-
-  {
-    double* Bsh=(double*)ush;
-    const int rbc[6]={0,63,126,189,237,249};
-    int t = bx-13;
-    const int img = t/249; t -= img*249;
-    int lvl=0; while (lvl<4 && t>=rbc[lvl+1]) lvl++;
-    const int i0=(t-rbc[lvl])*32;
-    const int K=kl[lvl]; const int nw=(K+63)>>6;
-    const double* B=allB+(size_t)(img*TOTK+loff[lvl])*4;
-    for (int q=tid;q<K*4;q+=1024) Bsh[q]=B[q];
-    __syncthreads();
-    const int wv=tid>>6, lane=tid&63;
-    for (int rr=0;rr<32;rr++){
-      int i=i0+rr;
-      if (i>=K) break;
-      const double bi0=Bsh[i*4],bi1=Bsh[i*4+1],bi2=Bsh[i*4+2],bi3=Bsh[i*4+3];
-      const double areai=(bi2-bi0)*(bi3-bi1);
-      for (int w=wv;w<nw;w+=16){
-        int j=w*64+lane;
-        bool pred=false;
-        if (j<K && j!=i){
-          double a0=Bsh[j*4],a1=Bsh[j*4+1],a2=Bsh[j*4+2],a3=Bsh[j*4+3];
-          double lt0=fmax(bi0,a0), lt1=fmax(bi1,a1);
-          double rb0=fmin(bi2,a2), rb1=fmin(bi3,a3);
-          double ww=rb0-lt0; if (ww<0.0) ww=0.0;
-          double hh=rb1-lt1; if (hh<0.0) hh=0.0;
-          double inter=ww*hh;
-          double uni=areai+(a2-a0)*(a3-a1)-inter;
-          double iou=inter>0.0?inter/uni:0.0;
-          pred = iou>0.7;
-        }
-        unsigned long long m=__ballot(pred);
-        if (lane==0) msk[((size_t)img*TOTK+loff[lvl]+i)*32+w]=m;
-      }
-    }
-    __syncthreads();
-    if (tid==0){ __threadfence(); atomicAdd(&flags[img*5+lvl],1); }
   }
 }
 
@@ -760,6 +791,7 @@
   unsigned long long* msk=(unsigned long long*)carve(2ull*TOTK*32*8);
   double* part   =(double*)carve(256*2*8);
   unsigned long long* keepbuf=(unsigned long long*)carve(2*124*8);
+  uint32_t* tfk  =(uint32_t*)carve(8*4);
   if ((size_t)(p-(char*)d_ws) > ws_size) return;
 
   hipMemsetAsync(highest, 0, 1024, stream);
@@ -767,19 +799,17 @@
   uint32_t a0,b0,a1,b1;
   threefry(0u,42u,0u,2u,&a0,&b0);
   threefry(0u,42u,1u,3u,&a1,&b1);
-  uint32_t kf00,kf01,kb00,kb01,kf10,kf11,kb10,kb11;
+  uint32_t hk[8];
   { uint32_t c0,d0,c1,d1;
     threefry(a0,a1,0u,2u,&c0,&d0); threefry(a0,a1,1u,3u,&c1,&d1);
-    kf00=c0; kf01=c1; kb00=d0; kb01=d1;
+    hk[0]=c0; hk[1]=c1; hk[2]=d0; hk[3]=d1;
     threefry(b0,b1,0u,2u,&c0,&d0); threefry(b0,b1,1u,3u,&c1,&d1);
-    kf10=c0; kf11=c1; kb10=d0; kb11=d1; }
-
-  k_pre<<<704, 256, 0, stream>>>(cw, cwTf, gt, highest);
-  k_conv_label<<<4775, 256, 0, stream>>>(feats[0],feats[1],feats[2],feats[3],feats[4],
+    hk[4]=c0; hk[5]=c1; hk[6]=d0; hk[7]=d1; }
+  hipMemcpyAsync(tfk, hk, 32, hipMemcpyHostToDevice, stream);
+
+  k_pre<<<704, 256, 0, stream>>>(cw, cwTf, gt, highest, keepbuf);
+  k_main<<<N_MAIN, 256, 0, stream>>>(feats[0],feats[1],feats[2],feats[3],feats[4],
       cwTf,cb,ow,ob,dwt,dbt, logits, dpred,
-      gt, highest, prelab, matched, labels, counts,
-      ub, kf00,kf01,kb00,kb01,kf10,kf11,kb10,kb11);
-  k_mid2<<<78, 1024, 0, stream>>>(ub, prelab, counts, labels, logits, dpred,
-      allS, allB, keepbuf, gt, matched, part, flags);
-  k_mid3post<<<511, 1024, 0, stream>>>(allB, msk, part, allS, flags, keepbuf, out);
-}
+      gt, highest, prelab, matched, labels, counts, ub, tfk,
+      allS, allB, msk, keepbuf, part, flags, out);
+}
```

Result: slower. 2.030 ms (+62.5%).
